# Kernel tuning notes

Measured on AMD Instinct MI355X. Metric: run time of the kernel, lower is better.

The kernel has to match this reference:

```python
import jax, jax.numpy as jnp
import numpy as np
import math

NUM_HEADS = 16
NUM_BUCKETS = 32
MAX_DISTANCE = 128
ALPHA = 32.0


def _rel_bucket(rel_pos):
    # bidirectional T5-style bucketing
    nb = NUM_BUCKETS // 2
    buckets = (rel_pos > 0).astype(jnp.int32) * nb
    rel_pos = jnp.abs(rel_pos)
    max_exact = nb // 2
    is_small = rel_pos < max_exact
    large = max_exact + (
        jnp.log(rel_pos.astype(jnp.float32) / max_exact + 1e-06)
        / math.log(MAX_DISTANCE / max_exact)
        * (nb - max_exact)
    ).astype(jnp.int32)
    large = jnp.minimum(large, nb - 1)
    return buckets + jnp.where(is_small, rel_pos, large)


def setup_inputs() -> dict:
    key = jax.random.key(0)
    ks = jax.random.split(key, 12)
    T, B, E = 1024, 4, 1024
    hd = E // NUM_HEADS
    s = 0.02
    f32 = jnp.float32
    return {
        "query": jax.random.normal(ks[0], (T, B, E), f32),
        "q_w": jax.random.normal(ks[1], (E, E), f32) * s,
        "q_b": jnp.zeros((E,), f32),
        "k_w": jax.random.normal(ks[2], (E, E), f32) * s,
        "k_b": jnp.zeros((E,), f32),
        "v_w": jax.random.normal(ks[3], (E, E), f32) * s,
        "v_b": jnp.zeros((E,), f32),
        "out_w": jax.random.normal(ks[4], (E, E), f32) * s,
        "out_b": jnp.zeros((E,), f32),
        "rel_emb": jax.random.normal(ks[5], (NUM_BUCKETS, NUM_HEADS), f32) * 0.1,
        "grep_w": jax.random.normal(ks[6], (hd, 8), f32) * s,
        "grep_b": jnp.zeros((8,), f32),
        "grep_a": jnp.ones((1, NUM_HEADS, 1, 1), f32),
        "bias_k": jax.random.normal(ks[7], (1, 1, E), f32) * s,
        "bias_v": jax.random.normal(ks[8], (1, 1, E), f32) * s,
    }


def reference(query, q_w, q_b, k_w, k_b, v_w, v_b, out_w, out_b,
              rel_emb, grep_w, grep_b, grep_a, bias_k, bias_v):
    tgt_len, bsz, embed_dim = query.shape
    nh = NUM_HEADS
    hd = embed_dim // nh
    scaling = hd ** (-0.5)

    # projections (self-attention: q, k, v all from query)
    q = query @ q_w + q_b
    k = query @ k_w + k_b
    v = query @ v_w + v_b
    q = q * scaling / ALPHA

    # bias_kv concat along sequence axis
    k = jnp.concatenate([k, jnp.tile(bias_k, (1, bsz, 1))], axis=0)
    v = jnp.concatenate([v, jnp.tile(bias_v, (1, bsz, 1))], axis=0)

    # faithful to source layout (including its (bsz,tgt,nh,hd)->(bsz*nh,tgt,hd) reshape)
    q = jnp.transpose(q.reshape(tgt_len, bsz, nh, hd), (1, 0, 2, 3)).reshape(bsz * nh, tgt_len, hd)
    k = jnp.transpose(k.reshape(-1, bsz, nh, hd), (1, 0, 2, 3)).reshape(bsz * nh, -1, hd)
    v = jnp.transpose(v.reshape(-1, bsz, nh, hd), (1, 0, 2, 3)).reshape(bsz * nh, -1, hd)
    src_len = k.shape[1]

    # [B*H, T, S]
    attn_weights = jnp.einsum("bth,bsh->bts", q, k)

    # T5-style relative position bias
    rel_pos = jnp.arange(src_len)[None, :] - jnp.arange(tgt_len)[:, None]
    buckets = _rel_bucket(rel_pos)                        # [T, S]
    pb = rel_emb[buckets]                                 # [T, S, H]
    pb = jnp.transpose(pb, (2, 0, 1))                     # [H, T, S]
    pb = jnp.tile(pb[None], (bsz, 1, 1, 1)).reshape(bsz * nh, tgt_len, src_len)

    # GRU-style gating of the position bias
    query_layer = q.reshape(bsz, nh, tgt_len, hd) * ALPHA / scaling
    gate = jax.nn.sigmoid((query_layer @ grep_w + grep_b).sum(-1, keepdims=True))
    gate = (gate * grep_a).reshape(bsz * nh, tgt_len, 1)
    attn_weights = attn_weights + gate * pb

    probs = jax.nn.softmax(attn_weights, axis=-1)
    attn = jnp.einsum("bts,bsh->bth", probs, v)           # [B*H, T, hd]
    attn = attn.reshape(bsz, nh, tgt_len, hd)
    attn = jnp.transpose(attn, (2, 0, 1, 3)).reshape(tgt_len, bsz, embed_dim)
    return attn @ out_w + out_b
```

## Files before the change

### kernel.cpp

```cpp
#include <hip/hip_runtime.h>
#include <stdint.h>

typedef unsigned short u16;
typedef __attribute__((ext_vector_type(4))) float  f32x4;
typedef __attribute__((ext_vector_type(8))) short  short8;
typedef __attribute__((ext_vector_type(8))) u16    u16x8;
typedef __attribute__((ext_vector_type(4))) u16    u16x4;
typedef __attribute__((ext_vector_type(4))) float  fv4;

#define T_LEN 1024
#define EMB   1024
#define SPAD  1088
#define M_ROWS 4096

#define OFF_QX   (0ull)
#define OFF_WT   (8388608ull)
#define OFF_QB   (16777216ull)
#define OFF_KB   (25165824ull)
#define OFF_VT   (34078720ull)
#define OFF_AT   (42991616ull)
#define OFF_GATE (51380224ull)
#define OFF_PB   (51642368ull)

__device__ __forceinline__ u16 f2bf(float f) {
  uint32_t u = __builtin_bit_cast(uint32_t, f);
  u += 0x7FFFu + ((u >> 16) & 1u);
  return (u16)(u >> 16);
}
__device__ __forceinline__ float bf2f(u16 s) {
  uint32_t u = ((uint32_t)s) << 16;
  return __builtin_bit_cast(float, u);
}
__device__ __forceinline__ void gld_lds16(const void* gp, void* lp) {
  __builtin_amdgcn_global_load_lds(
      (const __attribute__((address_space(1))) uint32_t*)(uintptr_t)(gp),
      (__attribute__((address_space(3))) uint32_t*)(uintptr_t)(lp),
      16, 0, 0);
}

__global__ void k_convert_q(const float* __restrict__ q, u16* __restrict__ qx) {
  int i = blockIdx.x * 256 + threadIdx.x;
  fv4 v = *((const fv4*)q + i);
  u16x4 o = { f2bf(v[0]), f2bf(v[1]), f2bf(v[2]), f2bf(v[3]) };
  *((u16x4*)qx + i) = o;
}

__global__ void k_transw(const float* __restrict__ w0, const float* __restrict__ w1,
                         const float* __restrict__ w2, const float* __restrict__ w3,
                         u16* __restrict__ wt) {
  __shared__ float tile[32][33];
  const int z = blockIdx.z;
  const float* w = (z == 0) ? w0 : (z == 1) ? w1 : (z == 2) ? w2 : w3;
  const int r0 = blockIdx.y * 32, c0 = blockIdx.x * 32;
  const int tx = threadIdx.x, ty = threadIdx.y;
  #pragma unroll
  for (int j = 0; j < 32; j += 8)
    tile[ty + j][tx] = w[(size_t)(r0 + ty + j) * EMB + c0 + tx];
  __syncthreads();
  u16* o = wt + (size_t)z * EMB * EMB;
  #pragma unroll
  for (int j = 0; j < 32; j += 8)
    o[(size_t)(c0 + ty + j) * EMB + r0 + tx] = f2bf(tile[tx][ty + j]);
}

__global__ void k_pb(const float* __restrict__ rel_emb, float* __restrict__ pbtab) {
  int i = blockIdx.x * 256 + threadIdx.x;
  int rel = i - 1023;
  int bucket = (rel > 0) ? 16 : 0;
  int r = rel < 0 ? -rel : rel;
  int bidx;
  if (r < 8) bidx = r;
  else {
    float lf = __logf((float)r / 8.0f + 1e-6f) * (1.0f / logf(16.0f)) * 8.0f;
    int large = 8 + (int)lf;
    bidx = large < 15 ? large : 15;
  }
  bucket += bidx;
  #pragma unroll
  for (int h = 0; h < 16; ++h) pbtab[h * 2048 + i] = rel_emb[bucket * 16 + h];
}

__device__ __forceinline__ void gemm_tile(const u16* __restrict__ A, const u16* __restrict__ Bt,
                                          int m0, int n0, u16* As, u16* Bs, f32x4 acc[4][4]) {
  const int tid = threadIdx.x;
  const int lane = tid & 63, wid = tid >> 6;
  const int wm = wid >> 1, wn = wid & 1;
  const int l15 = lane & 15, l4 = lane >> 4;
  for (int kt = 0; kt < EMB; kt += 32) {
    #pragma unroll
    for (int i = 0; i < 2; ++i) {
      int cw = wid * 64 + i * 256;
      int c = cw + lane;
      int row = c >> 2, cb = c & 3;
      gld_lds16(A  + (size_t)(m0 + row) * EMB + kt + cb * 8, (char*)As + (size_t)cw * 16);
      gld_lds16(Bt + (size_t)(n0 + row) * EMB + kt + cb * 8, (char*)Bs + (size_t)cw * 16);
    }
    __syncthreads();
    short8 a[4], b[4];
    #pragma unroll
    for (int f = 0; f < 4; ++f) {
      a[f] = *(const short8*)(As + (wm * 64 + f * 16 + l15) * 32 + l4 * 8);
      b[f] = *(const short8*)(Bs + (wn * 64 + f * 16 + l15) * 32 + l4 * 8);
    }
    #pragma unroll
    for (int mi = 0; mi < 4; ++mi)
      #pragma unroll
      for (int ni = 0; ni < 4; ++ni)
        acc[mi][ni] = __builtin_amdgcn_mfma_f32_16x16x32_bf16(a[mi], b[ni], acc[mi][ni], 0, 0, 0);
    __syncthreads();
  }
}

__global__ __launch_bounds__(256, 2) void k_qkv_gemm(const u16* __restrict__ qx, const u16* __restrict__ wt,
    const float* __restrict__ qbias, const float* __restrict__ kbias, const float* __restrict__ vbias,
    u16* __restrict__ qb, u16* __restrict__ kb, u16* __restrict__ vt) {
  __shared__ u16 lds[8192];
  const int z = blockIdx.z;
  f32x4 acc[4][4];
  #pragma unroll
  for (int i = 0; i < 4; ++i)
    #pragma unroll
    for (int j = 0; j < 4; ++j) acc[i][j] = (f32x4){0.f, 0.f, 0.f, 0.f};
  const int m0 = blockIdx.y * 128, n0 = blockIdx.x * 128;
  gemm_tile(qx, wt + (size_t)z * EMB * EMB, m0, n0, lds, lds + 4096, acc);
  const float* bias = (z == 0) ? qbias : (z == 1) ? kbias : vbias;
  const int lane = threadIdx.x & 63, wid = threadIdx.x >> 6;
  const int wm = wid >> 1, wn = wid & 1, l15 = lane & 15, l4 = lane >> 4;
  #pragma unroll
  for (int ni = 0; ni < 4; ++ni) {
    int col = n0 + wn * 64 + ni * 16 + l15;
    float bv = bias[col];
    int h = col >> 6, d = col & 63;
    #pragma unroll
    for (int mi = 0; mi < 4; ++mi) {
      #pragma unroll
      for (int r = 0; r < 4; ++r) {
        int row = m0 + wm * 64 + mi * 16 + l4 * 4 + r;
        int t = row >> 2, b = row & 3;
        float v = acc[mi][ni][r] + bv;
        if (z == 0) {
          int x = b * 16 + (t >> 6), u = ((t & 63) << 4) + h;
          qb[((size_t)x * 1024 + u) * 64 + d] = f2bf(v * (1.0f / 256.0f));
        } else {
          int w = t * 16 + h;
          int j = w / 1025;
          int u = w - j * 1025;
          int x = b * 16 + j;
          if (z == 1) kb[((size_t)x * SPAD + u) * 64 + d] = f2bf(v);
          else        vt[((size_t)x * 64 + d) * SPAD + u] = f2bf(v);
        }
      }
    }
  }
}

__global__ void k_biaskv(const float* __restrict__ bias_k, const float* __restrict__ bias_v,
                         u16* __restrict__ kb, u16* __restrict__ vt) {
  int i = blockIdx.x * 256 + threadIdx.x;
  int b = i >> 10, h = (i >> 6) & 15, d = i & 63;
  int x = b * 16 + 15, u = 1009 + h;
  kb[((size_t)x * SPAD + u) * 64 + d] = f2bf(bias_k[h * 64 + d]);
  vt[((size_t)x * 64 + d) * SPAD + u] = f2bf(bias_v[h * 64 + d]);
}

__global__ void k_gate(const u16* __restrict__ qb, const float* __restrict__ grep_w,
                       const float* __restrict__ grep_b, const float* __restrict__ grep_a,
                       float* __restrict__ gate) {
  int lane = threadIdx.x & 63, wid = threadIdx.x >> 6;
  int item = blockIdx.x * 4 + wid;
  int x = item >> 10;
  float wg = 0.f, bg = 0.f;
  #pragma unroll
  for (int j = 0; j < 8; ++j) { wg += grep_w[lane * 8 + j]; bg += grep_b[j]; }
  float qv = bf2f(qb[(size_t)item * 64 + lane]) * 256.0f;
  float v = qv * wg;
  #pragma unroll
  for (int mk = 32; mk; mk >>= 1) v += __shfl_xor(v, mk);
  if (lane == 0) {
    float s = 1.0f / (1.0f + __expf(-(v + bg)));
    gate[item] = s * grep_a[x & 15];
  }
}

__global__ __launch_bounds__(256, 2) void k_attn(const u16* __restrict__ qb, const u16* __restrict__ kb,
    const u16* __restrict__ vt, const float* __restrict__ gate, const float* __restrict__ pbt,
    u16* __restrict__ at) {
  __shared__ float pb_s[2048];
  __shared__ u16 Qs[128 * 72];
  __shared__ u16 Ks[64 * 72];
  __shared__ u16 Vs[64 * 72];
  __shared__ u16 Ps[4][32 * 72];
  const int tid = threadIdx.x, lane = tid & 63, wid = tid >> 6;
  const int l15 = lane & 15, l4 = lane >> 4;
  const int x = blockIdx.y, h = x & 15, b = x >> 4;
  const int t0 = blockIdx.x * 128;

  #pragma unroll
  for (int i = 0; i < 2; ++i) {
    int idx = (tid + i * 256) * 4;
    *(fv4*)(pb_s + idx) = *(const fv4*)(pbt + (size_t)h * 2048 + idx);
  }
  #pragma unroll
  for (int i = 0; i < 4; ++i) {
    int c = tid + i * 256, row = c >> 3, cb = c & 7;
    *(u16x8*)(&Qs[row * 72 + cb * 8]) =
        *(const u16x8*)(qb + ((size_t)x * 1024 + t0 + row) * 64 + cb * 8);
  }
  float g[2][4];
  #pragma unroll
  for (int mf = 0; mf < 2; ++mf)
    #pragma unroll
    for (int r = 0; r < 4; ++r)
      g[mf][r] = gate[(size_t)x * 1024 + t0 + wid * 32 + mf * 16 + l4 * 4 + r];

  float m_[2][4], l_[2][4];
  f32x4 O[2][4];
  #pragma unroll
  for (int mf = 0; mf < 2; ++mf)
    #pragma unroll
    for (int r = 0; r < 4; ++r) { m_[mf][r] = -1e30f; l_[mf][r] = 0.f; }
  #pragma unroll
  for (int mf = 0; mf < 2; ++mf)
    #pragma unroll
    for (int df = 0; df < 4; ++df) O[mf][df] = (f32x4){0.f, 0.f, 0.f, 0.f};

  __syncthreads();

  short8 qa[2][2];
  #pragma unroll
  for (int mf = 0; mf < 2; ++mf)
    #pragma unroll
    for (int ks = 0; ks < 2; ++ks)
      qa[mf][ks] = *(const short8*)(&Qs[(wid * 32 + mf * 16 + l15) * 72 + l4 * 8 + ks * 32]);

  for (int ic = 0; ic < 17; ++ic) {
    const int s0 = ic * 64;
    #pragma unroll
    for (int i = 0; i < 2; ++i) {
      int c = tid + i * 256, row = c >> 3, cb = c & 7;
      *(u16x8*)(&Ks[row * 72 + cb * 8]) =
          *(const u16x8*)(kb + ((size_t)x * SPAD + s0 + row) * 64 + cb * 8);
      *(u16x8*)(&Vs[row * 72 + cb * 8]) =
          *(const u16x8*)(vt + ((size_t)x * 64 + row) * SPAD + s0 + cb * 8);
    }
    __syncthreads();
    short8 kf[4][2];
    #pragma unroll
    for (int nf = 0; nf < 4; ++nf)
      #pragma unroll
      for (int ks = 0; ks < 2; ++ks)
        kf[nf][ks] = *(const short8*)(&Ks[(nf * 16 + l15) * 72 + l4 * 8 + ks * 32]);
    f32x4 sc[2][4];
    #pragma unroll
    for (int mf = 0; mf < 2; ++mf)
      #pragma unroll
      for (int nf = 0; nf < 4; ++nf) sc[mf][nf] = (f32x4){0.f, 0.f, 0.f, 0.f};
    #pragma unroll
    for (int mf = 0; mf < 2; ++mf)
      #pragma unroll
      for (int nf = 0; nf < 4; ++nf)
        #pragma unroll
        for (int ks = 0; ks < 2; ++ks)
          sc[mf][nf] = __builtin_amdgcn_mfma_f32_16x16x32_bf16(qa[mf][ks], kf[nf][ks], sc[mf][nf], 0, 0, 0);
    #pragma unroll
    for (int mf = 0; mf < 2; ++mf) {
      #pragma unroll
      for (int nf = 0; nf < 4; ++nf) {
        #pragma unroll
        for (int r = 0; r < 4; ++r) {
          int t = t0 + wid * 32 + mf * 16 + l4 * 4 + r;
          int s = s0 + nf * 16 + l15;
          int ridx = s - t + 1023;
          float pbv = pb_s[ridx < 2047 ? ridx : 2047];
          float v = sc[mf][nf][r] + g[mf][r] * pbv;
          sc[mf][nf][r] = (s <= 1024) ? v : -1e30f;
        }
      }
    }
    #pragma unroll
    for (int mf = 0; mf < 2; ++mf) {
      #pragma unroll
      for (int r = 0; r < 4; ++r) {
        float rm = fmaxf(fmaxf(sc[mf][0][r], sc[mf][1][r]), fmaxf(sc[mf][2][r], sc[mf][3][r]));
        rm = fmaxf(rm, __shfl_xor(rm, 1));
        rm = fmaxf(rm, __shfl_xor(rm, 2));
        rm = fmaxf(rm, __shfl_xor(rm, 4));
        rm = fmaxf(rm, __shfl_xor(rm, 8));
        float mo = m_[mf][r];
        float mn = fmaxf(mo, rm);
        float cf = __expf(mo - mn);
        m_[mf][r] = mn;
        float rs = 0.f;
        #pragma unroll
        for (int nf = 0; nf < 4; ++nf) {
          float p = __expf(sc[mf][nf][r] - mn);
          sc[mf][nf][r] = p;
          rs += p;
        }
        rs += __shfl_xor(rs, 1);
        rs += __shfl_xor(rs, 2);
        rs += __shfl_xor(rs, 4);
        rs += __shfl_xor(rs, 8);
        l_[mf][r] = l_[mf][r] * cf + rs;
        #pragma unroll
        for (int df = 0; df < 4; ++df) O[mf][df][r] *= cf;
      }
    }
    u16* Pw = Ps[wid];
    #pragma unroll
    for (int mf = 0; mf < 2; ++mf)
      #pragma unroll
      for (int nf = 0; nf < 4; ++nf)
        #pragma unroll
        for (int r = 0; r < 4; ++r)
          Pw[(mf * 16 + l4 * 4 + r) * 72 + nf * 16 + l15] = f2bf(sc[mf][nf][r]);
    __asm__ volatile("s_waitcnt lgkmcnt(0)" ::: "memory");
    __builtin_amdgcn_sched_barrier(0);
    short8 pa[2][2], vb[4][2];
    #pragma unroll
    for (int mf = 0; mf < 2; ++mf)
      #pragma unroll
      for (int ks = 0; ks < 2; ++ks)
        pa[mf][ks] = *(const short8*)(&Pw[(mf * 16 + l15) * 72 + l4 * 8 + ks * 32]);
    #pragma unroll
    for (int df = 0; df < 4; ++df)
      #pragma unroll
      for (int ks = 0; ks < 2; ++ks)
        vb[df][ks] = *(const short8*)(&Vs[(df * 16 + l15) * 72 + l4 * 8 + ks * 32]);
    #pragma unroll
    for (int mf = 0; mf < 2; ++mf)
      #pragma unroll
      for (int df = 0; df < 4; ++df)
        #pragma unroll
        for (int ks = 0; ks < 2; ++ks)
          O[mf][df] = __builtin_amdgcn_mfma_f32_16x16x32_bf16(pa[mf][ks], vb[df][ks], O[mf][df], 0, 0, 0);
    __syncthreads();
  }
  #pragma unroll
  for (int mf = 0; mf < 2; ++mf) {
    #pragma unroll
    for (int df = 0; df < 4; ++df) {
      #pragma unroll
      for (int r = 0; r < 4; ++r) {
        int t = t0 + wid * 32 + mf * 16 + l4 * 4 + r;
        int col = h * 64 + df * 16 + l15;
        float o = O[mf][df][r] / l_[mf][r];
        at[((size_t)(t * 4 + b)) * 1024 + col] = f2bf(o);
      }
    }
  }
}

__global__ __launch_bounds__(256, 2) void k_out_gemm(const u16* __restrict__ at, const u16* __restrict__ wt3,
                                                     const float* __restrict__ obias, float* __restrict__ out) {
  __shared__ u16 lds[8192];
  f32x4 acc[4][4];
  #pragma unroll
  for (int i = 0; i < 4; ++i)
    #pragma unroll
    for (int j = 0; j < 4; ++j) acc[i][j] = (f32x4){0.f, 0.f, 0.f, 0.f};
  const int m0 = blockIdx.y * 128, n0 = blockIdx.x * 128;
  gemm_tile(at, wt3, m0, n0, lds, lds + 4096, acc);
  const int lane = threadIdx.x & 63, wid = threadIdx.x >> 6;
  const int wm = wid >> 1, wn = wid & 1, l15 = lane & 15, l4 = lane >> 4;
  #pragma unroll
  for (int ni = 0; ni < 4; ++ni) {
    int col = n0 + wn * 64 + ni * 16 + l15;
    float bv = obias[col];
    #pragma unroll
    for (int mi = 0; mi < 4; ++mi) {
      #pragma unroll
      for (int r = 0; r < 4; ++r) {
        int row = m0 + wm * 64 + mi * 16 + l4 * 4 + r;
        out[(size_t)row * 1024 + col] = acc[mi][ni][r] + bv;
      }
    }
  }
}

extern "C" void kernel_launch(void* const* d_in, const int* in_sizes, int n_in,
                              void* d_out, int out_size, void* d_ws, size_t ws_size,
                              hipStream_t stream) {
  const float* query   = (const float*)d_in[0];
  const float* q_w     = (const float*)d_in[1];
  const float* q_b     = (const float*)d_in[2];
  const float* k_w     = (const float*)d_in[3];
  const float* k_b     = (const float*)d_in[4];
  const float* v_w     = (const float*)d_in[5];
  const float* v_b     = (const float*)d_in[6];
  const float* out_w   = (const float*)d_in[7];
  const float* out_b   = (const float*)d_in[8];
  const float* rel_emb = (const float*)d_in[9];
  const float* grep_w  = (const float*)d_in[10];
  const float* grep_b  = (const float*)d_in[11];
  const float* grep_a  = (const float*)d_in[12];
  const float* bias_k  = (const float*)d_in[13];
  const float* bias_v  = (const float*)d_in[14];
  char* ws = (char*)d_ws;
  u16*   qx  = (u16*)(ws + OFF_QX);
  u16*   wt  = (u16*)(ws + OFF_WT);
  u16*   qb  = (u16*)(ws + OFF_QB);
  u16*   kb  = (u16*)(ws + OFF_KB);
  u16*   vt  = (u16*)(ws + OFF_VT);
  u16*   at  = (u16*)(ws + OFF_AT);
  float* gate = (float*)(ws + OFF_GATE);
  float* pbt  = (float*)(ws + OFF_PB);
  float* out  = (float*)d_out;

  k_convert_q<<<dim3(4096), dim3(256), 0, stream>>>(query, qx);
  k_transw<<<dim3(32, 32, 4), dim3(32, 8), 0, stream>>>(q_w, k_w, v_w, out_w, wt);
  k_pb<<<dim3(8), dim3(256), 0, stream>>>(rel_emb, pbt);
  k_qkv_gemm<<<dim3(8, 32, 3), dim3(256), 0, stream>>>(qx, wt, q_b, k_b, v_b, qb, kb, vt);
  k_biaskv<<<dim3(16), dim3(256), 0, stream>>>(bias_k, bias_v, kb, vt);
  k_gate<<<dim3(16384), dim3(256), 0, stream>>>(qb, grep_w, grep_b, grep_a, gate);
  k_attn<<<dim3(8, 64), dim3(256), 0, stream>>>(qb, kb, vt, gate, pbt, at);
  k_out_gemm<<<dim3(8, 32), dim3(256), 0, stream>>>(at, wt + (size_t)3 * EMB * EMB, out_b, out);
}
```

Before: 256.3 us.

## Restructure attention to 8 waves per block with exp2 softmax and peeled tail

Attention now runs 512-thread blocks where each wave owns 16 query rows instead of 32, and a 1D grid with a swizzled block index replaces the 2D grid. The P tile is staged into the already-consumed Q region of shared memory, and the padded 17th key chunk is replaced by 16 full chunks plus a single peeled bias_kv column, which drops the per-element masking. Log2(e) is folded into the Q scaling and the bias table so the softmax can use exp2. The gate kernel is rewritten so each wave covers 8 rows using precomputed grep sums. Smaller per-wave tiles lower register use and raise occupancy, at the cost of less reuse of K and V fragments per wave.

```diff
diff --git a/kernel.cpp b/kernel.cpp
--- a/kernel.cpp
+++ b/kernel.cpp
@@ -11,7 +11,7 @@
 #define T_LEN 1024
 #define EMB   1024
 #define SPAD  1088
-#define M_ROWS 4096
+#define LOG2E 1.44269504f
 
 #define OFF_QX   (0ull)
 #define OFF_WT   (8388608ull)
@@ -63,7 +63,9 @@
     o[(size_t)(c0 + ty + j) * EMB + r0 + tx] = f2bf(tile[tx][ty + j]);
 }
 
-__global__ void k_pb(const float* __restrict__ rel_emb, float* __restrict__ pbtab) {
+__global__ void k_pb(const float* __restrict__ rel_emb, float* __restrict__ pbtab,
+                     const float* __restrict__ grep_w, const float* __restrict__ grep_b,
+                     float* __restrict__ aux) {
   int i = blockIdx.x * 256 + threadIdx.x;
   int rel = i - 1023;
   int bucket = (rel > 0) ? 16 : 0;
@@ -77,7 +79,20 @@
   }
   bucket += bidx;
   #pragma unroll
-  for (int h = 0; h < 16; ++h) pbtab[h * 2048 + i] = rel_emb[bucket * 16 + h];
+  for (int h = 0; h < 16; ++h) pbtab[h * 2048 + i] = rel_emb[bucket * 16 + h] * LOG2E;
+  if (blockIdx.x == 0) {
+    if (threadIdx.x < 64) {
+      float s = 0.f;
+      #pragma unroll
+      for (int j = 0; j < 8; ++j) s += grep_w[threadIdx.x * 8 + j];
+      aux[threadIdx.x] = s;
+    } else if (threadIdx.x == 64) {
+      float s = 0.f;
+      #pragma unroll
+      for (int j = 0; j < 8; ++j) s += grep_b[j];
+      aux[64] = s;
+    }
+  }
 }
 
 __device__ __forceinline__ void gemm_tile(const u16* __restrict__ A, const u16* __restrict__ Bt,
@@ -140,7 +155,7 @@
         float v = acc[mi][ni][r] + bv;
         if (z == 0) {
           int x = b * 16 + (t >> 6), u = ((t & 63) << 4) + h;
-          qb[((size_t)x * 1024 + u) * 64 + d] = f2bf(v * (1.0f / 256.0f));
+          qb[((size_t)x * 1024 + u) * 64 + d] = f2bf(v * (LOG2E / 256.0f));
         } else {
           int w = t * 16 + h;
           int j = w / 1025;
@@ -163,190 +178,181 @@
   vt[((size_t)x * 64 + d) * SPAD + u] = f2bf(bias_v[h * 64 + d]);
 }
 
-__global__ void k_gate(const u16* __restrict__ qb, const float* __restrict__ grep_w,
-                       const float* __restrict__ grep_b, const float* __restrict__ grep_a,
-                       float* __restrict__ gate) {
-  int lane = threadIdx.x & 63, wid = threadIdx.x >> 6;
-  int item = blockIdx.x * 4 + wid;
-  int x = item >> 10;
-  float wg = 0.f, bg = 0.f;
-  #pragma unroll
-  for (int j = 0; j < 8; ++j) { wg += grep_w[lane * 8 + j]; bg += grep_b[j]; }
-  float qv = bf2f(qb[(size_t)item * 64 + lane]) * 256.0f;
-  float v = qv * wg;
-  #pragma unroll
-  for (int mk = 32; mk; mk >>= 1) v += __shfl_xor(v, mk);
-  if (lane == 0) {
-    float s = 1.0f / (1.0f + __expf(-(v + bg)));
-    gate[item] = s * grep_a[x & 15];
-  }
-}
-
-__global__ __launch_bounds__(256, 2) void k_attn(const u16* __restrict__ qb, const u16* __restrict__ kb,
+__global__ void k_gate(const u16* __restrict__ qb, const float* __restrict__ aux,
+                       const float* __restrict__ grep_a, float* __restrict__ gate) {
+  int tid = threadIdx.x, lane = tid & 63, wid = tid >> 6;
+  int row0 = (blockIdx.x * 4 + wid) * 8;
+  int sub = lane >> 3, d0 = (lane & 7) * 8;
+  int item = row0 + sub;
+  u16x8 q8 = *(const u16x8*)(qb + (size_t)item * 64 + d0);
+  float acc = 0.f;
+  #pragma unroll
+  for (int j = 0; j < 8; ++j) acc += bf2f(q8[j]) * aux[d0 + j];
+  acc += __shfl_xor(acc, 1);
+  acc += __shfl_xor(acc, 2);
+  acc += __shfl_xor(acc, 4);
+  if ((lane & 7) == 0) {
+    float v = acc * (256.0f / LOG2E) + aux[64];
+    float s = 1.0f / (1.0f + __expf(-v));
+    gate[item] = s * grep_a[(item >> 10) & 15];
+  }
+}
+
+__global__ __launch_bounds__(512, 4) void k_attn(const u16* __restrict__ qb, const u16* __restrict__ kb,
     const u16* __restrict__ vt, const float* __restrict__ gate, const float* __restrict__ pbt,
     u16* __restrict__ at) {
   __shared__ float pb_s[2048];
   __shared__ u16 Qs[128 * 72];
   __shared__ u16 Ks[64 * 72];
   __shared__ u16 Vs[64 * 72];
-  __shared__ u16 Ps[4][32 * 72];
   const int tid = threadIdx.x, lane = tid & 63, wid = tid >> 6;
   const int l15 = lane & 15, l4 = lane >> 4;
-  const int x = blockIdx.y, h = x & 15, b = x >> 4;
-  const int t0 = blockIdx.x * 128;
-
+  const int bid = blockIdx.x;
+  const int x = (bid & 7) + ((bid >> 6) << 3);
+  const int tblk = (bid >> 3) & 7;
+  const int h = x & 15, b = x >> 4;
+  const int t0 = tblk * 128;
+
+  *(fv4*)(pb_s + tid * 4) = *(const fv4*)(pbt + (size_t)h * 2048 + tid * 4);
   #pragma unroll
   for (int i = 0; i < 2; ++i) {
-    int idx = (tid + i * 256) * 4;
-    *(fv4*)(pb_s + idx) = *(const fv4*)(pbt + (size_t)h * 2048 + idx);
-  }
-  #pragma unroll
-  for (int i = 0; i < 4; ++i) {
-    int c = tid + i * 256, row = c >> 3, cb = c & 7;
+    int c = tid + i * 512, row = c >> 3, cb = c & 7;
     *(u16x8*)(&Qs[row * 72 + cb * 8]) =
         *(const u16x8*)(qb + ((size_t)x * 1024 + t0 + row) * 64 + cb * 8);
   }
-  float g[2][4];
-  #pragma unroll
-  for (int mf = 0; mf < 2; ++mf)
-    #pragma unroll
-    for (int r = 0; r < 4; ++r)
-      g[mf][r] = gate[(size_t)x * 1024 + t0 + wid * 32 + mf * 16 + l4 * 4 + r];
-
-  float m_[2][4], l_[2][4];
-  f32x4 O[2][4];
-  #pragma unroll
-  for (int mf = 0; mf < 2; ++mf)
-    #pragma unroll
-    for (int r = 0; r < 4; ++r) { m_[mf][r] = -1e30f; l_[mf][r] = 0.f; }
-  #pragma unroll
-  for (int mf = 0; mf < 2; ++mf)
-    #pragma unroll
-    for (int df = 0; df < 4; ++df) O[mf][df] = (f32x4){0.f, 0.f, 0.f, 0.f};
+  const int trow = t0 + wid * 16 + l4 * 4;
+  float g[4];
+  #pragma unroll
+  for (int r = 0; r < 4; ++r)
+    g[r] = gate[(size_t)x * 1024 + trow + r];
+
+  float m_[4], l_[4];
+  f32x4 O[4];
+  #pragma unroll
+  for (int r = 0; r < 4; ++r) { m_[r] = -1e30f; l_[r] = 0.f; }
+  #pragma unroll
+  for (int df = 0; df < 4; ++df) O[df] = (f32x4){0.f, 0.f, 0.f, 0.f};
 
   __syncthreads();
 
-  short8 qa[2][2];
-  #pragma unroll
-  for (int mf = 0; mf < 2; ++mf)
-    #pragma unroll
-    for (int ks = 0; ks < 2; ++ks)
-      qa[mf][ks] = *(const short8*)(&Qs[(wid * 32 + mf * 16 + l15) * 72 + l4 * 8 + ks * 32]);
-
-  for (int ic = 0; ic < 17; ++ic) {
+  short8 qa[2];
+  #pragma unroll
+  for (int ks = 0; ks < 2; ++ks)
+    qa[ks] = *(const short8*)(&Qs[(wid * 16 + l15) * 72 + ks * 32 + l4 * 8]);
+  u16* Pw = &Qs[wid * 16 * 72];
+
+  for (int ic = 0; ic < 16; ++ic) {
     const int s0 = ic * 64;
-    #pragma unroll
-    for (int i = 0; i < 2; ++i) {
-      int c = tid + i * 256, row = c >> 3, cb = c & 7;
+    {
+      int row = tid >> 3, cb = tid & 7;
       *(u16x8*)(&Ks[row * 72 + cb * 8]) =
           *(const u16x8*)(kb + ((size_t)x * SPAD + s0 + row) * 64 + cb * 8);
       *(u16x8*)(&Vs[row * 72 + cb * 8]) =
           *(const u16x8*)(vt + ((size_t)x * 64 + row) * SPAD + s0 + cb * 8);
     }
     __syncthreads();
-    short8 kf[4][2];
+    f32x4 sc[4];
+    #pragma unroll
+    for (int nf = 0; nf < 4; ++nf) {
+      sc[nf] = (f32x4){0.f, 0.f, 0.f, 0.f};
+      short8 k0 = *(const short8*)(&Ks[(nf * 16 + l15) * 72 + l4 * 8]);
+      short8 k1 = *(const short8*)(&Ks[(nf * 16 + l15) * 72 + 32 + l4 * 8]);
+      sc[nf] = __builtin_amdgcn_mfma_f32_16x16x32_bf16(qa[0], k0, sc[nf], 0, 0, 0);
+      sc[nf] = __builtin_amdgcn_mfma_f32_16x16x32_bf16(qa[1], k1, sc[nf], 0, 0, 0);
+    }
+    #pragma unroll
+    for (int nf = 0; nf < 4; ++nf) {
+      int s = s0 + nf * 16 + l15;
+      #pragma unroll
+      for (int r = 0; r < 4; ++r) {
+        int ridx = s - (trow + r) + 1023;
+        sc[nf][r] = sc[nf][r] + g[r] * pb_s[ridx];
+      }
+    }
+    #pragma unroll
+    for (int r = 0; r < 4; ++r) {
+      float rm = fmaxf(fmaxf(sc[0][r], sc[1][r]), fmaxf(sc[2][r], sc[3][r]));
+      rm = fmaxf(rm, __shfl_xor(rm, 1));
+      rm = fmaxf(rm, __shfl_xor(rm, 2));
+      rm = fmaxf(rm, __shfl_xor(rm, 4));
+      rm = fmaxf(rm, __shfl_xor(rm, 8));
+      float mo = m_[r];
+      float mn = fmaxf(mo, rm);
+      float cf = exp2f(mo - mn);
+      m_[r] = mn;
+      float rs = 0.f;
+      #pragma unroll
+      for (int nf = 0; nf < 4; ++nf) {
+        float p = exp2f(sc[nf][r] - mn);
+        sc[nf][r] = p;
+        rs += p;
+      }
+      rs += __shfl_xor(rs, 1);
+      rs += __shfl_xor(rs, 2);
+      rs += __shfl_xor(rs, 4);
+      rs += __shfl_xor(rs, 8);
+      l_[r] = l_[r] * cf + rs;
+      #pragma unroll
+      for (int df = 0; df < 4; ++df) O[df][r] *= cf;
+    }
     #pragma unroll
     for (int nf = 0; nf < 4; ++nf)
       #pragma unroll
-      for (int ks = 0; ks < 2; ++ks)
-        kf[nf][ks] = *(const short8*)(&Ks[(nf * 16 + l15) * 72 + l4 * 8 + ks * 32]);
-    f32x4 sc[2][4];
-    #pragma unroll
-    for (int mf = 0; mf < 2; ++mf)
-      #pragma unroll
-      for (int nf = 0; nf < 4; ++nf) sc[mf][nf] = (f32x4){0.f, 0.f, 0.f, 0.f};
-    #pragma unroll
-    for (int mf = 0; mf < 2; ++mf)
-      #pragma unroll
-      for (int nf = 0; nf < 4; ++nf)
-        #pragma unroll
-        for (int ks = 0; ks < 2; ++ks)
-          sc[mf][nf] = __builtin_amdgcn_mfma_f32_16x16x32_bf16(qa[mf][ks], kf[nf][ks], sc[mf][nf], 0, 0, 0);
-    #pragma unroll
-    for (int mf = 0; mf < 2; ++mf) {
-      #pragma unroll
-      for (int nf = 0; nf < 4; ++nf) {
-        #pragma unroll
-        for (int r = 0; r < 4; ++r) {
-          int t = t0 + wid * 32 + mf * 16 + l4 * 4 + r;
-          int s = s0 + nf * 16 + l15;
-          int ridx = s - t + 1023;
-          float pbv = pb_s[ridx < 2047 ? ridx : 2047];
-          float v = sc[mf][nf][r] + g[mf][r] * pbv;
-          sc[mf][nf][r] = (s <= 1024) ? v : -1e30f;
-        }
-      }
-    }
-    #pragma unroll
-    for (int mf = 0; mf < 2; ++mf) {
-      #pragma unroll
-      for (int r = 0; r < 4; ++r) {
-        float rm = fmaxf(fmaxf(sc[mf][0][r], sc[mf][1][r]), fmaxf(sc[mf][2][r], sc[mf][3][r]));
-        rm = fmaxf(rm, __shfl_xor(rm, 1));
-        rm = fmaxf(rm, __shfl_xor(rm, 2));
-        rm = fmaxf(rm, __shfl_xor(rm, 4));
-        rm = fmaxf(rm, __shfl_xor(rm, 8));
-        float mo = m_[mf][r];
-        float mn = fmaxf(mo, rm);
-        float cf = __expf(mo - mn);
-        m_[mf][r] = mn;
-        float rs = 0.f;
-        #pragma unroll
-        for (int nf = 0; nf < 4; ++nf) {
-          float p = __expf(sc[mf][nf][r] - mn);
-          sc[mf][nf][r] = p;
-          rs += p;
-        }
-        rs += __shfl_xor(rs, 1);
-        rs += __shfl_xor(rs, 2);
-        rs += __shfl_xor(rs, 4);
-        rs += __shfl_xor(rs, 8);
-        l_[mf][r] = l_[mf][r] * cf + rs;
-        #pragma unroll
-        for (int df = 0; df < 4; ++df) O[mf][df][r] *= cf;
-      }
-    }
-    u16* Pw = Ps[wid];
-    #pragma unroll
-    for (int mf = 0; mf < 2; ++mf)
-      #pragma unroll
-      for (int nf = 0; nf < 4; ++nf)
-        #pragma unroll
-        for (int r = 0; r < 4; ++r)
-          Pw[(mf * 16 + l4 * 4 + r) * 72 + nf * 16 + l15] = f2bf(sc[mf][nf][r]);
+      for (int r = 0; r < 4; ++r)
+        Pw[(l4 * 4 + r) * 72 + nf * 16 + l15] = f2bf(sc[nf][r]);
     __asm__ volatile("s_waitcnt lgkmcnt(0)" ::: "memory");
     __builtin_amdgcn_sched_barrier(0);
-    short8 pa[2][2], vb[4][2];
-    #pragma unroll
-    for (int mf = 0; mf < 2; ++mf)
-      #pragma unroll
-      for (int ks = 0; ks < 2; ++ks)
-        pa[mf][ks] = *(const short8*)(&Pw[(mf * 16 + l15) * 72 + l4 * 8 + ks * 32]);
-    #pragma unroll
-    for (int df = 0; df < 4; ++df)
-      #pragma unroll
-      for (int ks = 0; ks < 2; ++ks)
-        vb[df][ks] = *(const short8*)(&Vs[(df * 16 + l15) * 72 + l4 * 8 + ks * 32]);
-    #pragma unroll
-    for (int mf = 0; mf < 2; ++mf)
-      #pragma unroll
-      for (int df = 0; df < 4; ++df)
-        #pragma unroll
-        for (int ks = 0; ks < 2; ++ks)
-          O[mf][df] = __builtin_amdgcn_mfma_f32_16x16x32_bf16(pa[mf][ks], vb[df][ks], O[mf][df], 0, 0, 0);
+    short8 pa[2];
+    #pragma unroll
+    for (int ks = 0; ks < 2; ++ks)
+      pa[ks] = *(const short8*)(&Pw[l15 * 72 + ks * 32 + l4 * 8]);
+    #pragma unroll
+    for (int df = 0; df < 4; ++df) {
+      short8 v0 = *(const short8*)(&Vs[(df * 16 + l15) * 72 + l4 * 8]);
+      short8 v1 = *(const short8*)(&Vs[(df * 16 + l15) * 72 + 32 + l4 * 8]);
+      O[df] = __builtin_amdgcn_mfma_f32_16x16x32_bf16(pa[0], v0, O[df], 0, 0, 0);
+      O[df] = __builtin_amdgcn_mfma_f32_16x16x32_bf16(pa[1], v1, O[df], 0, 0, 0);
+    }
     __syncthreads();
   }
-  #pragma unroll
-  for (int mf = 0; mf < 2; ++mf) {
-    #pragma unroll
-    for (int df = 0; df < 4; ++df) {
-      #pragma unroll
-      for (int r = 0; r < 4; ++r) {
-        int t = t0 + wid * 32 + mf * 16 + l4 * 4 + r;
-        int col = h * 64 + df * 16 + l15;
-        float o = O[mf][df][r] / l_[mf][r];
-        at[((size_t)(t * 4 + b)) * 1024 + col] = f2bf(o);
-      }
+
+  if (tid < 128) {
+    int row = tid >> 3, cb = tid & 7;
+    *(u16x8*)(&Ks[row * 72 + cb * 8]) =
+        *(const u16x8*)(kb + ((size_t)x * SPAD + 1024 + row) * 64 + cb * 8);
+  }
+  __syncthreads();
+  f32x4 sc0 = (f32x4){0.f, 0.f, 0.f, 0.f};
+  {
+    short8 k0 = *(const short8*)(&Ks[l15 * 72 + l4 * 8]);
+    short8 k1 = *(const short8*)(&Ks[l15 * 72 + 32 + l4 * 8]);
+    sc0 = __builtin_amdgcn_mfma_f32_16x16x32_bf16(qa[0], k0, sc0, 0, 0, 0);
+    sc0 = __builtin_amdgcn_mfma_f32_16x16x32_bf16(qa[1], k1, sc0, 0, 0, 0);
+  }
+  float vtail[4];
+  #pragma unroll
+  for (int df = 0; df < 4; ++df)
+    vtail[df] = bf2f(vt[((size_t)x * 64 + df * 16 + l15) * SPAD + 1024]);
+  #pragma unroll
+  for (int r = 0; r < 4; ++r) {
+    int t = trow + r;
+    float dotv = __shfl(sc0[r], lane & 48);
+    float se = dotv + g[r] * pb_s[2047 - t];
+    float mn = fmaxf(m_[r], se);
+    float cf = exp2f(m_[r] - mn);
+    float pe = exp2f(se - mn);
+    l_[r] = l_[r] * cf + pe;
+    #pragma unroll
+    for (int df = 0; df < 4; ++df) O[df][r] = O[df][r] * cf + pe * vtail[df];
+  }
+
+  #pragma unroll
+  for (int df = 0; df < 4; ++df) {
+    #pragma unroll
+    for (int r = 0; r < 4; ++r) {
+      int t = trow + r;
+      int col = h * 64 + df * 16 + l15;
+      at[((size_t)(t * 4 + b)) * 1024 + col] = f2bf(O[df][r] / l_[r]);
     }
   }
 }
@@ -403,16 +409,17 @@
   u16*   kb  = (u16*)(ws + OFF_KB);
   u16*   vt  = (u16*)(ws + OFF_VT);
   u16*   at  = (u16*)(ws + OFF_AT);
+  float* aux = (float*)(ws + OFF_AT);
   float* gate = (float*)(ws + OFF_GATE);
   float* pbt  = (float*)(ws + OFF_PB);
   float* out  = (float*)d_out;
 
   k_convert_q<<<dim3(4096), dim3(256), 0, stream>>>(query, qx);
   k_transw<<<dim3(32, 32, 4), dim3(32, 8), 0, stream>>>(q_w, k_w, v_w, out_w, wt);
-  k_pb<<<dim3(8), dim3(256), 0, stream>>>(rel_emb, pbt);
+  k_pb<<<dim3(8), dim3(256), 0, stream>>>(rel_emb, pbt, grep_w, grep_b, aux);
   k_qkv_gemm<<<dim3(8, 32, 3), dim3(256), 0, stream>>>(qx, wt, q_b, k_b, v_b, qb, kb, vt);
   k_biaskv<<<dim3(16), dim3(256), 0, stream>>>(bias_k, bias_v, kb, vt);
-  k_gate<<<dim3(16384), dim3(256), 0, stream>>>(qb, grep_w, grep_b, grep_a, gate);
-  k_attn<<<dim3(8, 64), dim3(256), 0, stream>>>(qb, kb, vt, gate, pbt, at);
+  k_gate<<<dim3(2048), dim3(256), 0, stream>>>(qb, aux, grep_a, gate);
+  k_attn<<<dim3(512), dim3(512), 0, stream>>>(qb, kb, vt, gate, pbt, at);
   k_out_gemm<<<dim3(8, 32), dim3(256), 0, stream>>>(at, wt + (size_t)3 * EMB * EMB, out_b, out);
 }
```

After: 249.2 us. 2.8% less time.
